# Kernel tuning notes

Hardware: AMD Instinct MI355X
Metric: run time of the kernel (lower is better)

The kernel has to match this reference:

```python
import jax, jax.numpy as jnp
import numpy as np

USER_NUM = 100000
ITEM_NUM = 50000
N_NODES = USER_NUM + ITEM_NUM
EMB = 128
N_EDGES = 600000
N_LAYERS = 3


def setup_inputs() -> dict:
    key = jax.random.key(0)
    k1, k2, k3, k4, k5 = jax.random.split(key, 5)
    user_emb = jax.random.normal(k1, (USER_NUM, EMB), dtype=jnp.float32) * 0.05
    item_emb = jax.random.normal(k2, (ITEM_NUM, EMB), dtype=jnp.float32) * 0.05
    edge_row = jax.random.randint(k3, (N_EDGES,), 0, N_NODES, dtype=jnp.int32)
    edge_col = jax.random.randint(k4, (N_EDGES,), 0, N_NODES, dtype=jnp.int32)
    # symmetric-normalized adjacency values (positive, ~1/deg scale)
    edge_vals = jax.random.uniform(k5, (N_EDGES,), dtype=jnp.float32) * 0.1
    return {
        "user_emb": user_emb,
        "item_emb": item_emb,
        "edge_vals": edge_vals,
        "edge_row": edge_row,
        "edge_col": edge_col,
    }


def _spmm(edge_vals, edge_row, edge_col, x):
    # torch.sparse.mm(A, x) with A in COO form: out[r] += v * x[c]
    gathered = edge_vals[:, None] * x[edge_col]  # [E, D]
    return jax.ops.segment_sum(gathered, edge_row, num_segments=N_NODES)


def reference(user_emb, item_emb, edge_vals, edge_row, edge_col):
    ego = jnp.concatenate([user_emb, item_emb], axis=0)  # [N, D]
    acc = jnp.zeros_like(ego)
    for _ in range(N_LAYERS):
        ego = _spmm(edge_vals, edge_row, edge_col, ego)
        acc = acc + ego  # fused running sum instead of stack+mean
    all_embeddings = acc / N_LAYERS
    user_all = all_embeddings[:USER_NUM]
    item_all = all_embeddings[USER_NUM:]
    return (user_all, item_all)
```

## Files before the change

### kernel.cpp

```cpp
#include <hip/hip_runtime.h>

constexpr int USER_NUM = 100000;
constexpr int ITEM_NUM = 50000;
constexpr int N_NODES  = USER_NUM + ITEM_NUM;
constexpr int EMB      = 128;
constexpr int N_EDGES  = 600000;
constexpr int SCAN_BS  = 1024;

constexpr int EBLOCKS = (N_EDGES + 255) / 256;

typedef float vf4 __attribute__((ext_vector_type(4)));

__device__ __forceinline__ float bf2f(unsigned u16) {
    return __uint_as_float(u16 << 16);
}
__device__ __forceinline__ unsigned f2bf(float f) {
    unsigned u = __float_as_uint(f);
    u += 0x7fffu + ((u >> 16) & 1u);
    return u >> 16;
}
__device__ __forceinline__ void fmadd_bf8(float* s, float v, uint4 g) {
    s[0] += v * bf2f(g.x & 0xffffu);
    s[1] += v * bf2f(g.x >> 16);
    s[2] += v * bf2f(g.y & 0xffffu);
    s[3] += v * bf2f(g.y >> 16);
    s[4] += v * bf2f(g.z & 0xffffu);
    s[5] += v * bf2f(g.z >> 16);
    s[6] += v * bf2f(g.w & 0xffffu);
    s[7] += v * bf2f(g.w >> 16);
}

__global__ void hist_rank_k(const int* __restrict__ er, int* __restrict__ cnt,
                            int* __restrict__ rank) {
    int e = blockIdx.x * 256 + threadIdx.x;
    if (e < N_EDGES) rank[e] = atomicAdd(&cnt[er[e]], 1);
}

__global__ __launch_bounds__(SCAN_BS) void scan_fused_k(
        const int* __restrict__ cnt, int* __restrict__ gcount,
        int2* __restrict__ rowinfo) {
    __shared__ int sh[SCAN_BS];
    __shared__ int sbase;
    int i = blockIdx.x * SCAN_BS + threadIdx.x;
    int v = (i < N_NODES) ? cnt[i] : 0;
    sh[threadIdx.x] = v;
    __syncthreads();
    for (int off = 1; off < SCAN_BS; off <<= 1) {
        int t = (threadIdx.x >= off) ? sh[threadIdx.x - off] : 0;
        __syncthreads();
        sh[threadIdx.x] += t;
        __syncthreads();
    }
    if (threadIdx.x == SCAN_BS - 1)
        sbase = atomicAdd(gcount, sh[SCAN_BS - 1]);
    __syncthreads();
    if (i < N_NODES)
        rowinfo[i] = make_int2(sbase + sh[threadIdx.x] - v, v);
}

__global__ void scatter_k(const int* __restrict__ er, const int* __restrict__ ec,
                          const float* __restrict__ ev, const int* __restrict__ rank,
                          const int2* __restrict__ rowinfo, int2* __restrict__ edges) {
    int e = blockIdx.x * 256 + threadIdx.x;
    if (e >= N_EDGES) return;
    int p = rowinfo[er[e]].x + rank[e];
    edges[p] = make_int2(ec[e], __float_as_int(ev[e]));
}

__global__ __launch_bounds__(256) void spmm_l1_fp32(
        const float* __restrict__ ue, const float* __restrict__ ie,
        const int2* __restrict__ rowinfo, const int2* __restrict__ edges,
        uint4* __restrict__ out) {
    int row  = blockIdx.x * 16 + (threadIdx.x >> 4);
    int lane = threadIdx.x & 15;
    int2 ri = rowinfo[row];
    int e0 = ri.x, eend = ri.x + ri.y;
    float s[8] = {0.f, 0.f, 0.f, 0.f, 0.f, 0.f, 0.f, 0.f};
    for (int base = e0; base < eend; base += 4) {
        int i1 = (base + 1 < eend) ? base + 1 : eend - 1;
        int i2 = (base + 2 < eend) ? base + 2 : eend - 1;
        int i3 = (base + 3 < eend) ? base + 3 : eend - 1;
        int2 p0 = edges[base], p1 = edges[i1], p2 = edges[i2], p3 = edges[i3];
        float v0 = __int_as_float(p0.y);
        float v1 = (base + 1 < eend) ? __int_as_float(p1.y) : 0.f;
        float v2 = (base + 2 < eend) ? __int_as_float(p2.y) : 0.f;
        float v3 = (base + 3 < eend) ? __int_as_float(p3.y) : 0.f;
        const vf4* s0 = (const vf4*)((p0.x < USER_NUM) ? ue + (size_t)p0.x * EMB
                                     : ie + (size_t)(p0.x - USER_NUM) * EMB);
        const vf4* s1 = (const vf4*)((p1.x < USER_NUM) ? ue + (size_t)p1.x * EMB
                                     : ie + (size_t)(p1.x - USER_NUM) * EMB);
        const vf4* s2 = (const vf4*)((p2.x < USER_NUM) ? ue + (size_t)p2.x * EMB
                                     : ie + (size_t)(p2.x - USER_NUM) * EMB);
        const vf4* s3 = (const vf4*)((p3.x < USER_NUM) ? ue + (size_t)p3.x * EMB
                                     : ie + (size_t)(p3.x - USER_NUM) * EMB);
        vf4 a0 = s0[lane * 2], b0 = s0[lane * 2 + 1];
        vf4 a1 = s1[lane * 2], b1 = s1[lane * 2 + 1];
        vf4 a2 = s2[lane * 2], b2 = s2[lane * 2 + 1];
        vf4 a3 = s3[lane * 2], b3 = s3[lane * 2 + 1];
        s[0] += v0 * a0.x; s[1] += v0 * a0.y; s[2] += v0 * a0.z; s[3] += v0 * a0.w;
        s[4] += v0 * b0.x; s[5] += v0 * b0.y; s[6] += v0 * b0.z; s[7] += v0 * b0.w;
        s[0] += v1 * a1.x; s[1] += v1 * a1.y; s[2] += v1 * a1.z; s[3] += v1 * a1.w;
        s[4] += v1 * b1.x; s[5] += v1 * b1.y; s[6] += v1 * b1.z; s[7] += v1 * b1.w;
        s[0] += v2 * a2.x; s[1] += v2 * a2.y; s[2] += v2 * a2.z; s[3] += v2 * a2.w;
        s[4] += v2 * b2.x; s[5] += v2 * b2.y; s[6] += v2 * b2.z; s[7] += v2 * b2.w;
        s[0] += v3 * a3.x; s[1] += v3 * a3.y; s[2] += v3 * a3.z; s[3] += v3 * a3.w;
        s[4] += v3 * b3.x; s[5] += v3 * b3.y; s[6] += v3 * b3.z; s[7] += v3 * b3.w;
    }
    uint4 w;
    w.x = f2bf(s[0]) | (f2bf(s[1]) << 16);
    w.y = f2bf(s[2]) | (f2bf(s[3]) << 16);
    w.z = f2bf(s[4]) | (f2bf(s[5]) << 16);
    w.w = f2bf(s[6]) | (f2bf(s[7]) << 16);
    out[(size_t)row * 16 + lane] = w;
}

template <int MODE>
__global__ __launch_bounds__(256) void spmm_gather_bf(
        const uint4* __restrict__ x, const int2* __restrict__ rowinfo,
        const int2* __restrict__ edges, uint4* __restrict__ out,
        const uint4* __restrict__ b0, float* __restrict__ acc) {
    int row  = blockIdx.x * 16 + (threadIdx.x >> 4);
    int lane = threadIdx.x & 15;
    int2 ri = rowinfo[row];
    int e0 = ri.x, eend = ri.x + ri.y;
    float s[8] = {0.f, 0.f, 0.f, 0.f, 0.f, 0.f, 0.f, 0.f};
    for (int base = e0; base < eend; base += 4) {
        int i1 = (base + 1 < eend) ? base + 1 : eend - 1;
        int i2 = (base + 2 < eend) ? base + 2 : eend - 1;
        int i3 = (base + 3 < eend) ? base + 3 : eend - 1;
        int2 p0 = edges[base], p1 = edges[i1], p2 = edges[i2], p3 = edges[i3];
        float v0 = __int_as_float(p0.y);
        float v1 = (base + 1 < eend) ? __int_as_float(p1.y) : 0.f;
        float v2 = (base + 2 < eend) ? __int_as_float(p2.y) : 0.f;
        float v3 = (base + 3 < eend) ? __int_as_float(p3.y) : 0.f;
        uint4 g0 = x[(size_t)p0.x * 16 + lane];
        uint4 g1 = x[(size_t)p1.x * 16 + lane];
        uint4 g2 = x[(size_t)p2.x * 16 + lane];
        uint4 g3 = x[(size_t)p3.x * 16 + lane];
        fmadd_bf8(s, v0, g0);
        fmadd_bf8(s, v1, g1);
        fmadd_bf8(s, v2, g2);
        fmadd_bf8(s, v3, g3);
    }
    size_t o = (size_t)row * 16 + lane;
    if (MODE < 2) {
        uint4 w;
        w.x = f2bf(s[0]) | (f2bf(s[1]) << 16);
        w.y = f2bf(s[2]) | (f2bf(s[3]) << 16);
        w.z = f2bf(s[4]) | (f2bf(s[5]) << 16);
        w.w = f2bf(s[6]) | (f2bf(s[7]) << 16);
        out[o] = w;
    } else {
        uint4 a0 = b0[o];
        uint4 a1 = x[o];
        const float k = 1.0f / 3.0f;
        vf4 r0, r1;
        r0.x = (s[0] + bf2f(a0.x & 0xffffu) + bf2f(a1.x & 0xffffu)) * k;
        r0.y = (s[1] + bf2f(a0.x >> 16)     + bf2f(a1.x >> 16))     * k;
        r0.z = (s[2] + bf2f(a0.y & 0xffffu) + bf2f(a1.y & 0xffffu)) * k;
        r0.w = (s[3] + bf2f(a0.y >> 16)     + bf2f(a1.y >> 16))     * k;
        r1.x = (s[4] + bf2f(a0.z & 0xffffu) + bf2f(a1.z & 0xffffu)) * k;
        r1.y = (s[5] + bf2f(a0.z >> 16)     + bf2f(a1.z >> 16))     * k;
        r1.z = (s[6] + bf2f(a0.w & 0xffffu) + bf2f(a1.w & 0xffffu)) * k;
        r1.w = (s[7] + bf2f(a0.w >> 16)     + bf2f(a1.w >> 16))     * k;
        vf4* dst = reinterpret_cast<vf4*>(acc) + (size_t)row * 32 + (size_t)lane * 2;
        __builtin_nontemporal_store(r0, dst);
        __builtin_nontemporal_store(r1, dst + 1);
    }
}

__global__ void spmm_first_at(const float* __restrict__ ue, const float* __restrict__ ie,
                              const float* __restrict__ ev, const int* __restrict__ er,
                              const int* __restrict__ ec, float* __restrict__ out) {
    int tid = blockIdx.x * blockDim.x + threadIdx.x;
    int edge = tid >> 5;
    if (edge >= N_EDGES) return;
    int lane = tid & 31;
    int row = er[edge]; int col = ec[edge]; float v = ev[edge];
    const float* x = (col < USER_NUM) ? (ue + (size_t)col * EMB)
                                      : (ie + (size_t)(col - USER_NUM) * EMB);
    float4 g = ((const float4*)x)[lane];
    float* o = out + (size_t)row * EMB + lane * 4;
    atomicAdd(o + 0, v * g.x); atomicAdd(o + 1, v * g.y);
    atomicAdd(o + 2, v * g.z); atomicAdd(o + 3, v * g.w);
}
__global__ void spmm_at(const float* __restrict__ x, const float* __restrict__ ev,
                        const int* __restrict__ er, const int* __restrict__ ec,
                        float* __restrict__ out) {
    int tid = blockIdx.x * blockDim.x + threadIdx.x;
    int edge = tid >> 5;
    if (edge >= N_EDGES) return;
    int lane = tid & 31;
    int row = er[edge]; int col = ec[edge]; float v = ev[edge];
    float4 g = ((const float4*)(x + (size_t)col * EMB))[lane];
    float* o = out + (size_t)row * EMB + lane * 4;
    atomicAdd(o + 0, v * g.x); atomicAdd(o + 1, v * g.y);
    atomicAdd(o + 2, v * g.z); atomicAdd(o + 3, v * g.w);
}
__global__ void acc_add(float* __restrict__ acc, const float* __restrict__ cur,
                        float scale, int n4) {
    int i = blockIdx.x * blockDim.x + threadIdx.x;
    if (i >= n4) return;
    float4 a = ((const float4*)acc)[i];
    float4 c = ((const float4*)cur)[i];
    a.x = (a.x + c.x) * scale; a.y = (a.y + c.y) * scale;
    a.z = (a.z + c.z) * scale; a.w = (a.w + c.w) * scale;
    ((float4*)acc)[i] = a;
}

extern "C" void kernel_launch(void* const* d_in, const int* in_sizes, int n_in,
                              void* d_out, int out_size, void* d_ws, size_t ws_size,
                              hipStream_t stream) {
    const float* ue = (const float*)d_in[0];
    const float* ie = (const float*)d_in[1];
    const float* ev = (const float*)d_in[2];
    const int*   er = (const int*)d_in[3];
    const int*   ec = (const int*)d_in[4];
    float* acc = (float*)d_out;

    size_t nnodes16 = (size_t)N_NODES * 16;

    uint4* e1b  = (uint4*)d_ws;
    uint4* e2b  = e1b + nnodes16;
    int*   cnt  = (int*)(e2b + nnodes16);
    int*   gcount = cnt + N_NODES;
    int2*  rowinfo = (int2*)(gcount + 1);
    int*   rank = (int*)(rowinfo + N_NODES);
    int2*  edges = (int2*)(rank + N_EDGES);
    size_t needed = (char*)(edges + N_EDGES) - (char*)d_ws;

    const int BLOCK = 256;
    const int nscan = (N_NODES + SCAN_BS - 1) / SCAN_BS;

    if (ws_size >= needed) {
        (void)hipMemsetAsync(cnt, 0, ((size_t)N_NODES + 1) * sizeof(int), stream);
        hist_rank_k<<<EBLOCKS, BLOCK, 0, stream>>>(er, cnt, rank);
        scan_fused_k<<<nscan, SCAN_BS, 0, stream>>>(cnt, gcount, rowinfo);
        scatter_k<<<EBLOCKS, BLOCK, 0, stream>>>(er, ec, ev, rank, rowinfo, edges);

        const int gblocks = N_NODES / 16;
        spmm_l1_fp32<<<gblocks, BLOCK, 0, stream>>>(
            ue, ie, rowinfo, edges, e1b);
        spmm_gather_bf<1><<<gblocks, BLOCK, 0, stream>>>(
            e1b, rowinfo, edges, e2b, nullptr, nullptr);
        spmm_gather_bf<2><<<gblocks, BLOCK, 0, stream>>>(
            e2b, rowinfo, edges, nullptr, e1b, acc);
    } else {
        size_t nfloats = (size_t)N_NODES * EMB;
        float* buf0 = (float*)d_ws;
        float* buf1 = buf0 + nfloats;
        const int spmm_blocks = (N_EDGES * 32) / BLOCK;
        const int n4 = (int)(nfloats / 4);
        const int add_blocks = (n4 + BLOCK - 1) / BLOCK;
        (void)hipMemsetAsync(acc, 0, nfloats * sizeof(float), stream);
        (void)hipMemsetAsync(buf0, 0, nfloats * sizeof(float), stream);
        spmm_first_at<<<spmm_blocks, BLOCK, 0, stream>>>(ue, ie, ev, er, ec, buf0);
        acc_add<<<add_blocks, BLOCK, 0, stream>>>(acc, buf0, 1.0f, n4);
        (void)hipMemsetAsync(buf1, 0, nfloats * sizeof(float), stream);
        spmm_at<<<spmm_blocks, BLOCK, 0, stream>>>(buf0, ev, er, ec, buf1);
        acc_add<<<add_blocks, BLOCK, 0, stream>>>(acc, buf1, 1.0f, n4);
        (void)hipMemsetAsync(buf0, 0, nfloats * sizeof(float), stream);
        spmm_at<<<spmm_blocks, BLOCK, 0, stream>>>(buf1, ev, er, ec, buf0);
        acc_add<<<add_blocks, BLOCK, 0, stream>>>(acc, buf0, 1.0f / 3.0f, n4);
    }
}
```

Before: 298.3 us.

## Fuse CSR build kernels into one persistent kernel with grid barriers

Replaces the histogram, scan and scatter kernels with a single persistent kernel of 256 blocks x 1024 threads that separates the phases with software grid barriers on an atomic counter. Edges are processed four at a time through int4/float4 loads. The aim is to remove two kernel launches and the gaps between them. The cost is a spin-wait barrier that assumes all 256 blocks are co-resident, and a deadlock risk if they are not.

```diff
diff --git a/kernel.cpp b/kernel.cpp
--- a/kernel.cpp
+++ b/kernel.cpp
@@ -5,9 +5,10 @@
 constexpr int N_NODES  = USER_NUM + ITEM_NUM;
 constexpr int EMB      = 128;
 constexpr int N_EDGES  = 600000;
-constexpr int SCAN_BS  = 1024;
-
-constexpr int EBLOCKS = (N_EDGES + 255) / 256;
+
+constexpr int CSR_G   = 256;
+constexpr int CSR_B   = 1024;
+constexpr int NSCAN   = (N_NODES + CSR_B - 1) / CSR_B;
 
 typedef float vf4 __attribute__((ext_vector_type(4)));
 
@@ -30,41 +31,69 @@
     s[7] += v * bf2f(g.w >> 16);
 }
 
-__global__ void hist_rank_k(const int* __restrict__ er, int* __restrict__ cnt,
-                            int* __restrict__ rank) {
-    int e = blockIdx.x * 256 + threadIdx.x;
-    if (e < N_EDGES) rank[e] = atomicAdd(&cnt[er[e]], 1);
-}
-
-__global__ __launch_bounds__(SCAN_BS) void scan_fused_k(
-        const int* __restrict__ cnt, int* __restrict__ gcount,
-        int2* __restrict__ rowinfo) {
-    __shared__ int sh[SCAN_BS];
+__device__ __forceinline__ void grid_bar(int* bar, int target) {
+    __syncthreads();
+    if (threadIdx.x == 0) {
+        __threadfence();
+        __hip_atomic_fetch_add(bar, 1, __ATOMIC_RELEASE, __HIP_MEMORY_SCOPE_AGENT);
+        while (__hip_atomic_load(bar, __ATOMIC_ACQUIRE, __HIP_MEMORY_SCOPE_AGENT) < target)
+            __builtin_amdgcn_s_sleep(8);
+        __threadfence();
+    }
+    __syncthreads();
+}
+
+__global__ __launch_bounds__(CSR_B) void csr_build_k(
+        const int* __restrict__ er, const int* __restrict__ ec,
+        const float* __restrict__ ev,
+        int* __restrict__ cnt, int* __restrict__ gcount, int* bar,
+        int* __restrict__ rank, int2* __restrict__ rowinfo,
+        int2* __restrict__ edges) {
+    __shared__ int sh[CSR_B];
     __shared__ int sbase;
-    int i = blockIdx.x * SCAN_BS + threadIdx.x;
-    int v = (i < N_NODES) ? cnt[i] : 0;
-    sh[threadIdx.x] = v;
-    __syncthreads();
-    for (int off = 1; off < SCAN_BS; off <<= 1) {
-        int t = (threadIdx.x >= off) ? sh[threadIdx.x - off] : 0;
+    const int nthreads = CSR_G * CSR_B;
+    const int tid = blockIdx.x * CSR_B + threadIdx.x;
+
+    for (int i = tid; i < N_EDGES / 4; i += nthreads) {
+        int4 r4 = ((const int4*)er)[i];
+        int4 k4;
+        k4.x = atomicAdd(&cnt[r4.x], 1);
+        k4.y = atomicAdd(&cnt[r4.y], 1);
+        k4.z = atomicAdd(&cnt[r4.z], 1);
+        k4.w = atomicAdd(&cnt[r4.w], 1);
+        ((int4*)rank)[i] = k4;
+    }
+    grid_bar(bar, CSR_G);
+
+    if (blockIdx.x < NSCAN) {
+        int i = blockIdx.x * CSR_B + threadIdx.x;
+        int v = (i < N_NODES) ? cnt[i] : 0;
+        sh[threadIdx.x] = v;
         __syncthreads();
-        sh[threadIdx.x] += t;
+        for (int off = 1; off < CSR_B; off <<= 1) {
+            int t = (threadIdx.x >= off) ? sh[threadIdx.x - off] : 0;
+            __syncthreads();
+            sh[threadIdx.x] += t;
+            __syncthreads();
+        }
+        if (threadIdx.x == CSR_B - 1)
+            sbase = atomicAdd(gcount, sh[CSR_B - 1]);
         __syncthreads();
-    }
-    if (threadIdx.x == SCAN_BS - 1)
-        sbase = atomicAdd(gcount, sh[SCAN_BS - 1]);
-    __syncthreads();
-    if (i < N_NODES)
-        rowinfo[i] = make_int2(sbase + sh[threadIdx.x] - v, v);
-}
-
-__global__ void scatter_k(const int* __restrict__ er, const int* __restrict__ ec,
-                          const float* __restrict__ ev, const int* __restrict__ rank,
-                          const int2* __restrict__ rowinfo, int2* __restrict__ edges) {
-    int e = blockIdx.x * 256 + threadIdx.x;
-    if (e >= N_EDGES) return;
-    int p = rowinfo[er[e]].x + rank[e];
-    edges[p] = make_int2(ec[e], __float_as_int(ev[e]));
+        if (i < N_NODES)
+            rowinfo[i] = make_int2(sbase + sh[threadIdx.x] - v, v);
+    }
+    grid_bar(bar, 2 * CSR_G);
+
+    for (int i = tid; i < N_EDGES / 4; i += nthreads) {
+        int4 r4 = ((const int4*)er)[i];
+        int4 c4 = ((const int4*)ec)[i];
+        float4 v4 = ((const float4*)ev)[i];
+        int4 k4 = ((const int4*)rank)[i];
+        edges[rowinfo[r4.x].x + k4.x] = make_int2(c4.x, __float_as_int(v4.x));
+        edges[rowinfo[r4.y].x + k4.y] = make_int2(c4.y, __float_as_int(v4.y));
+        edges[rowinfo[r4.z].x + k4.z] = make_int2(c4.z, __float_as_int(v4.z));
+        edges[rowinfo[r4.w].x + k4.w] = make_int2(c4.w, __float_as_int(v4.w));
+    }
 }
 
 __global__ __launch_bounds__(256) void spmm_l1_fp32(
@@ -224,19 +253,18 @@
     uint4* e2b  = e1b + nnodes16;
     int*   cnt  = (int*)(e2b + nnodes16);
     int*   gcount = cnt + N_NODES;
-    int2*  rowinfo = (int2*)(gcount + 1);
+    int*   bar    = gcount + 1;
+    int2*  rowinfo = (int2*)(bar + 1);
     int*   rank = (int*)(rowinfo + N_NODES);
     int2*  edges = (int2*)(rank + N_EDGES);
     size_t needed = (char*)(edges + N_EDGES) - (char*)d_ws;
 
     const int BLOCK = 256;
-    const int nscan = (N_NODES + SCAN_BS - 1) / SCAN_BS;
 
     if (ws_size >= needed) {
-        (void)hipMemsetAsync(cnt, 0, ((size_t)N_NODES + 1) * sizeof(int), stream);
-        hist_rank_k<<<EBLOCKS, BLOCK, 0, stream>>>(er, cnt, rank);
-        scan_fused_k<<<nscan, SCAN_BS, 0, stream>>>(cnt, gcount, rowinfo);
-        scatter_k<<<EBLOCKS, BLOCK, 0, stream>>>(er, ec, ev, rank, rowinfo, edges);
+        (void)hipMemsetAsync(cnt, 0, ((size_t)N_NODES + 2) * sizeof(int), stream);
+        csr_build_k<<<CSR_G, CSR_B, 0, stream>>>(
+            er, ec, ev, cnt, gcount, bar, rank, rowinfo, edges);
 
         const int gblocks = N_NODES / 16;
         spmm_l1_fp32<<<gblocks, BLOCK, 0, stream>>>(
```

Result: slower. 360.7 us (+20.9%).
